# Optimization experiments

Hardware: AMD Instinct MI355X
Metric: run time of the kernel (lower is better)

Reference implementation:

```python
import jax, jax.numpy as jnp
import numpy as np

B, S, D, H = 4, 2048, 1024, 16
DK = D // H

def setup_inputs() -> dict:
    key = jax.random.key(0)
    ks = jax.random.split(key, 5)
    std = np.sqrt(2.0 / (D + D)).astype(np.float32)
    return {
        "x": jax.random.normal(ks[0], (B, S, D), dtype=jnp.float32),
        "W_q": jax.random.normal(ks[1], (D, D), dtype=jnp.float32) * std,
        "W_k": jax.random.normal(ks[2], (D, D), dtype=jnp.float32) * std,
        "W_v": jax.random.normal(ks[3], (D, D), dtype=jnp.float32) * std,
        "W_o": jax.random.normal(ks[4], (D, D), dtype=jnp.float32) * std,
    }

def reference(x, W_q, W_k, W_v, W_o):
    b, s, d = x.shape
    # Linear layers: y = x @ W.T  (W stored as [out, in])
    q = (x @ W_q.T).reshape(b, s, H, DK).transpose(0, 2, 1, 3)  # [b,h,s,dk]
    k = (x @ W_k.T).reshape(b, s, H, DK).transpose(0, 2, 1, 3)
    v = (x @ W_v.T).reshape(b, s, H, DK).transpose(0, 2, 1, 3)
    scale = 1.0 / jnp.sqrt(jnp.asarray(DK, dtype=x.dtype))
    scores = jnp.einsum("bhqd,bhkd->bhqk", q, k) * scale  # [b,h,s,s]
    causal = jnp.tril(jnp.ones((s, s), dtype=bool))
    scores = jnp.where(causal, scores, jnp.asarray(-jnp.inf, dtype=scores.dtype))
    attn = jax.nn.softmax(scores, axis=-1)
    out = jnp.einsum("bhqk,bhkd->bhqd", attn, v)  # [b,h,s,dk]
    out = out.transpose(0, 2, 1, 3).reshape(b, s, d)
    return out @ W_o.T
```

## Files before the change

### kernel.cpp

```cpp
#include <hip/hip_runtime.h>
#include <stdint.h>

#define B_  4
#define S_  2048
#define D_  1024
#define H_  16
#define DK_ 64
#define M_  (B_ * S_)

typedef __attribute__((ext_vector_type(4))) float  f32x4;
typedef __attribute__((ext_vector_type(8))) __bf16 bf16x8;
typedef __attribute__((ext_vector_type(4))) unsigned short us4;

__device__ __forceinline__ unsigned short cvt_bf16(float f) {
  unsigned u = __float_as_uint(f);
  return (unsigned short)((u + 0x7fffu + ((u >> 16) & 1u)) >> 16);
}

__device__ __forceinline__ f32x4 mfma16(bf16x8 a, bf16x8 b, f32x4 c) {
  return __builtin_amdgcn_mfma_f32_16x16x32_bf16(a, b, c, 0, 0, 0);
}

__device__ __forceinline__ void async16(const void* g, void* l) {
  __builtin_amdgcn_global_load_lds(
      (const __attribute__((address_space(1))) void*)g,
      (__attribute__((address_space(3))) void*)l, 16, 0, 0);
}

__global__ void cast_f32_bf16(const float* __restrict__ in,
                              unsigned short* __restrict__ out, int n4) {
  int i = blockIdx.x * blockDim.x + threadIdx.x;
  if (i >= n4) return;
  f32x4 v = ((const f32x4*)in)[i];
  us4 o;
  o[0] = cvt_bf16(v[0]); o[1] = cvt_bf16(v[1]);
  o[2] = cvt_bf16(v[2]); o[3] = cvt_bf16(v[3]);
  ((us4*)out)[i] = o;
}

template <int OUTMODE>
__global__ __launch_bounds__(256) void gemm_bt(
    const unsigned short* __restrict__ A,
    const unsigned short* __restrict__ Bm,
    void* __restrict__ Cp, int Mdim, int Ndim, int Kdim) {
  constexpr int BM = 128, BN = 128, BK = 32;
  __shared__ __align__(16) unsigned short As[BM * BK];
  __shared__ __align__(16) unsigned short Bs[BN * BK];

  const int tid = threadIdx.x;
  const int w = tid >> 6, l = tid & 63;
  const int l16 = l & 15, lg = l >> 4;
  const int wr = w >> 1, wc = w & 1;
  const int rowA0 = blockIdx.y * BM;
  const int rowB0 = blockIdx.x * BN;
  const int l4 = l >> 2;
  const int lk = (l & 3) * 8;

  f32x4 acc[4][4] = {};

  for (int kt = 0; kt < Kdim; kt += BK) {
#pragma unroll
    for (int j = 0; j < 2; ++j) {
      const int chunk = j * 4 + w;
      const int r = chunk * 16 + l4;
      async16(A  + (size_t)(rowA0 + r) * Kdim + kt + lk, &As[chunk * 512]);
      async16(Bm + (size_t)(rowB0 + r) * Kdim + kt + lk, &Bs[chunk * 512]);
    }
    __syncthreads();
    bf16x8 af[4], bfr[4];
#pragma unroll
    for (int m = 0; m < 4; ++m)
      af[m] = *(const bf16x8*)&As[(wr * 64 + m * 16 + l16) * BK + lg * 8];
#pragma unroll
    for (int n = 0; n < 4; ++n)
      bfr[n] = *(const bf16x8*)&Bs[(wc * 64 + n * 16 + l16) * BK + lg * 8];
#pragma unroll
    for (int m = 0; m < 4; ++m)
#pragma unroll
      for (int n = 0; n < 4; ++n)
        acc[m][n] = mfma16(af[m], bfr[n], acc[m][n]);
    __syncthreads();
  }

  const int rb = rowA0 + wr * 64;
  const int cb = rowB0 + wc * 64;
  if constexpr (OUTMODE == 2) {
    float* C = (float*)Cp;
#pragma unroll
    for (int m = 0; m < 4; ++m)
#pragma unroll
      for (int n = 0; n < 4; ++n) {
        const int r0 = rb + m * 16 + lg * 4;
        const int c0 = cb + n * 16 + l16;
#pragma unroll
        for (int j = 0; j < 4; ++j)
          C[(size_t)(r0 + j) * Ndim + c0] = acc[m][n][j];
      }
  } else if constexpr (OUTMODE == 0) {
    unsigned short* C = (unsigned short*)Cp;
#pragma unroll
    for (int m = 0; m < 4; ++m)
#pragma unroll
      for (int n = 0; n < 4; ++n) {
        const int r0 = rb + m * 16 + lg * 4;
        const int c0 = cb + n * 16 + l16;
#pragma unroll
        for (int j = 0; j < 4; ++j)
          C[(size_t)(r0 + j) * Ndim + c0] = cvt_bf16(acc[m][n][j]);
      }
  } else {
    unsigned short* C = (unsigned short*)Cp;
#pragma unroll
    for (int m = 0; m < 4; ++m)
#pragma unroll
      for (int n = 0; n < 4; ++n) {
        const int r0 = rb + m * 16 + lg * 4;
        const int c0 = cb + n * 16 + l16;
        us4 v;
#pragma unroll
        for (int j = 0; j < 4; ++j) v[j] = cvt_bf16(acc[m][n][j]);
        *(us4*)&C[((size_t)(r0 >> 11) * 1024 + c0) * 2048 + (r0 & 2047)] = v;
      }
  }
}


#define SMX(sc, mr, sr, oa, P, diag, rb, kv0)                                \
  do {                                                                       \
    _Pragma("unroll") for (int nc_ = 0; nc_ < 4; ++nc_)                      \
        _Pragma("unroll") for (int j_ = 0; j_ < 4; ++j_)                     \
            sc[nc_][j_] *= 0.125f;                                           \
    if (diag) {                                                              \
      _Pragma("unroll") for (int nc_ = 0; nc_ < 4; ++nc_) {                  \
        const int col_ = (kv0) + nc_ * 16 + l16;                             \
        _Pragma("unroll") for (int j_ = 0; j_ < 4; ++j_)                     \
            if (col_ > (rb) + j_) sc[nc_][j_] = -INFINITY;                   \
      }                                                                      \
    }                                                                        \
    _Pragma("unroll") for (int j_ = 0; j_ < 4; ++j_) {                       \
      float t_ = fmaxf(fmaxf(sc[0][j_], sc[1][j_]),                          \
                       fmaxf(sc[2][j_], sc[3][j_]));                         \
      t_ = fmaxf(t_, __shfl_xor(t_, 1));                                     \
      t_ = fmaxf(t_, __shfl_xor(t_, 2));                                     \
      t_ = fmaxf(t_, __shfl_xor(t_, 4));                                     \
      t_ = fmaxf(t_, __shfl_xor(t_, 8));                                     \
      const float mnew_ = fmaxf(mr[j_], t_);                                 \
      float rs_ = 0.f;                                                       \
      _Pragma("unroll") for (int nc_ = 0; nc_ < 4; ++nc_) {                  \
        const float p_ = __expf(sc[nc_][j_] - mnew_);                        \
        rs_ += p_;                                                           \
        P[lg * 4 + j_][nc_ * 16 + l16] = cvt_bf16(p_);                       \
      }                                                                      \
      rs_ += __shfl_xor(rs_, 1);                                             \
      rs_ += __shfl_xor(rs_, 2);                                             \
      rs_ += __shfl_xor(rs_, 4);                                             \
      rs_ += __shfl_xor(rs_, 8);                                             \
      const float al_ = __expf(mr[j_] - mnew_);                              \
      sr[j_] = sr[j_] * al_ + rs_;                                           \
      mr[j_] = mnew_;                                                        \
      _Pragma("unroll") for (int d_ = 0; d_ < 4; ++d_) oa[d_][j_] *= al_;    \
    }                                                                        \
  } while (0)

__global__ __launch_bounds__(256, 4) void flash_attn(
    const unsigned short* __restrict__ Q,
    const unsigned short* __restrict__ K,
    const unsigned short* __restrict__ Vt,
    unsigned short* __restrict__ O) {
  const int bid  = blockIdx.x;
  const int virt = (bid & 7) * 128 + (bid >> 3);
  const int bh   = virt >> 4;
  const int x    = virt & 15;
  const int b = bh >> 4, h = bh & 15;
  const int tid = threadIdx.x;
  const int w = tid >> 6, l = tid & 63;
  const int l16 = l & 15, lg = l >> 4;

  __shared__ __align__(16) unsigned short Ks[64 * 64];
  __shared__ __align__(16) unsigned short Vs[64 * 64];
  __shared__ __align__(16) unsigned short PA[4][16][72];
  __shared__ __align__(16) unsigned short PB[4][16][72];

  const int tA = x, tB = 31 - x;

  const size_t qkbase = (size_t)(b * S_) * D_ + h * DK_;
  const size_t vbase  = ((size_t)(b * D_) + h * DK_) * S_;

  const int rA = tA * 64 + w * 16 + l16;
  const int rB = tB * 64 + w * 16 + l16;
  bf16x8 qfA[2], qfB[2];
  qfA[0] = *(const bf16x8*)&Q[qkbase + (size_t)rA * D_ + lg * 8];
  qfA[1] = *(const bf16x8*)&Q[qkbase + (size_t)rA * D_ + 32 + lg * 8];
  qfB[0] = *(const bf16x8*)&Q[qkbase + (size_t)rB * D_ + lg * 8];
  qfB[1] = *(const bf16x8*)&Q[qkbase + (size_t)rB * D_ + 32 + lg * 8];

  float mA[4], sA[4], mB[4], sB[4];
  f32x4 oA[4] = {}, oB[4] = {};
#pragma unroll
  for (int j = 0; j < 4; ++j) {
    mA[j] = mB[j] = -INFINITY;
    sA[j] = sB[j] = 0.f;
  }

  const int rbA = tA * 64 + w * 16 + lg * 4;
  const int rbB = tB * 64 + w * 16 + lg * 4;

  for (int kv = 0; kv <= tB; ++kv) {
    const int kv0 = kv * 64;
    if (kv) __syncthreads();
#pragma unroll
    for (int c = 0; c < 2; ++c) {
      const int ci = c * 256 + w * 64;
      const int i  = ci + l;
      const int r  = i >> 3;
      const int cc = (i & 7) ^ (r & 7);
      async16(K  + qkbase + (size_t)(kv0 + r) * D_ + cc * 8, &Ks[ci * 8]);
      async16(Vt + vbase  + (size_t)r * S_ + kv0 + cc * 8,   &Vs[ci * 8]);
    }
    __syncthreads();

    if (kv <= tA) {
      f32x4 sc[4] = {};
#pragma unroll
      for (int nc = 0; nc < 4; ++nc) {
        const int r = nc * 16 + l16;
#pragma unroll
        for (int ks = 0; ks < 2; ++ks) {
          const int byte = (r * 128 + ks * 64 + lg * 16) ^ ((r & 7) << 4);
          bf16x8 kf = *(const bf16x8*)((const char*)Ks + byte);
          sc[nc] = mfma16(qfA[ks], kf, sc[nc]);
        }
      }
      SMX(sc, mA, sA, oA, PA[w], kv == tA, rbA, kv0);
      __asm__ volatile("s_waitcnt lgkmcnt(0)" ::: "memory");
      bf16x8 pa0 = *(const bf16x8*)&PA[w][l16][lg * 8];
      bf16x8 pa1 = *(const bf16x8*)&PA[w][l16][32 + lg * 8];
#pragma unroll
      for (int d = 0; d < 4; ++d) {
        const int r = d * 16 + l16;
#pragma unroll
        for (int ks = 0; ks < 2; ++ks) {
          const int byte = (r * 128 + ks * 64 + lg * 16) ^ ((r & 7) << 4);
          bf16x8 vf = *(const bf16x8*)((const char*)Vs + byte);
          oA[d] = mfma16(ks ? pa1 : pa0, vf, oA[d]);
        }
      }
    }

    {
      f32x4 sc[4] = {};
#pragma unroll
      for (int nc = 0; nc < 4; ++nc) {
        const int r = nc * 16 + l16;
#pragma unroll
        for (int ks = 0; ks < 2; ++ks) {
          const int byte = (r * 128 + ks * 64 + lg * 16) ^ ((r & 7) << 4);
          bf16x8 kf = *(const bf16x8*)((const char*)Ks + byte);
          sc[nc] = mfma16(qfB[ks], kf, sc[nc]);
        }
      }
      SMX(sc, mB, sB, oB, PB[w], kv == tB, rbB, kv0);
      __asm__ volatile("s_waitcnt lgkmcnt(0)" ::: "memory");
      bf16x8 pb0 = *(const bf16x8*)&PB[w][l16][lg * 8];
      bf16x8 pb1 = *(const bf16x8*)&PB[w][l16][32 + lg * 8];
#pragma unroll
      for (int d = 0; d < 4; ++d) {
        const int r = d * 16 + l16;
#pragma unroll
        for (int ks = 0; ks < 2; ++ks) {
          const int byte = (r * 128 + ks * 64 + lg * 16) ^ ((r & 7) << 4);
          bf16x8 vf = *(const bf16x8*)((const char*)Vs + byte);
          oB[d] = mfma16(ks ? pb1 : pb0, vf, oB[d]);
        }
      }
    }
  }

#pragma unroll
  for (int d = 0; d < 4; ++d)
#pragma unroll
    for (int j = 0; j < 4; ++j) {
      O[((size_t)(b * S_) + rbA + j) * D_ + h * DK_ + d * 16 + l16] =
          cvt_bf16(oA[d][j] / sA[j]);
      O[((size_t)(b * S_) + rbB + j) * D_ + h * DK_ + d * 16 + l16] =
          cvt_bf16(oB[d][j] / sB[j]);
    }
}

extern "C" void kernel_launch(void* const* d_in, const int* in_sizes, int n_in,
                              void* d_out, int out_size, void* d_ws,
                              size_t ws_size, hipStream_t stream) {
  const float* x  = (const float*)d_in[0];
  const float* Wq = (const float*)d_in[1];
  const float* Wk = (const float*)d_in[2];
  const float* Wv = (const float*)d_in[3];
  const float* Wo = (const float*)d_in[4];

  const size_t XN = (size_t)M_ * D_;
  const size_t WN = (size_t)D_ * D_;
  unsigned short* xb  = (unsigned short*)d_ws;
  unsigned short* Wqb = xb + XN;
  unsigned short* Wkb = Wqb + WN;
  unsigned short* Wvb = Wkb + WN;
  unsigned short* Wob = Wvb + WN;
  unsigned short* Qb  = Wob + WN;
  unsigned short* Kb  = Qb + XN;
  unsigned short* Vtb = Kb + XN;
  unsigned short* Ob  = Vtb + XN;

  cast_f32_bf16<<<(int)(XN / 4 / 256), 256, 0, stream>>>(x, xb, (int)(XN / 4));
  cast_f32_bf16<<<(int)(WN / 4 / 256), 256, 0, stream>>>(Wq, Wqb, (int)(WN / 4));
  cast_f32_bf16<<<(int)(WN / 4 / 256), 256, 0, stream>>>(Wk, Wkb, (int)(WN / 4));
  cast_f32_bf16<<<(int)(WN / 4 / 256), 256, 0, stream>>>(Wv, Wvb, (int)(WN / 4));
  cast_f32_bf16<<<(int)(WN / 4 / 256), 256, 0, stream>>>(Wo, Wob, (int)(WN / 4));

  dim3 gg(D_ / 128, M_ / 128);
  gemm_bt<0><<<gg, 256, 0, stream>>>(xb, Wqb, Qb, M_, D_, D_);
  gemm_bt<0><<<gg, 256, 0, stream>>>(xb, Wkb, Kb, M_, D_, D_);
  gemm_bt<1><<<gg, 256, 0, stream>>>(xb, Wvb, Vtb, M_, D_, D_);

  flash_attn<<<dim3(1024), 256, 0, stream>>>(Qb, Kb, Vtb, Ob);

  gemm_bt<2><<<gg, 256, 0, stream>>>(Ob, Wob, d_out, M_, D_, D_);
}
```

Measured before the change: 346.9 us.

## Fuse casts and QKV GEMMs, skip softmax rescale, use exp2 and setprio

Merges the five cast kernels into one launch and fuses the Q/K/V projections into a single GEMM over the concatenated weight matrix (N=3072), with the output routed per region. In flash attention, the 1/sqrt(dk) scale is folded into an exp2 constant, the rescale of the accumulator is skipped when the row max does not change (wave-uniform check), MFMA sections get raised wave priority, and the final division becomes a reciprocal multiply. The intent is to cut launch overhead, reuse x loads across the three projections, and trim softmax ALU work. The cost is extra branching and slightly different rounding.

```diff
diff --git a/kernel.cpp b/kernel.cpp
--- a/kernel.cpp
+++ b/kernel.cpp
@@ -27,22 +27,40 @@
       (__attribute__((address_space(3))) void*)l, 16, 0, 0);
 }
 
-__global__ void cast_f32_bf16(const float* __restrict__ in,
-                              unsigned short* __restrict__ out, int n4) {
-  int i = blockIdx.x * blockDim.x + threadIdx.x;
-  if (i >= n4) return;
-  f32x4 v = ((const f32x4*)in)[i];
+#define XN4_ 2097152
+#define WN4_ 262144
+__global__ void cast_all(const float* __restrict__ x,
+                         const float* __restrict__ wq,
+                         const float* __restrict__ wk,
+                         const float* __restrict__ wv,
+                         const float* __restrict__ wo,
+                         unsigned short* __restrict__ dst) {
+  const int i = blockIdx.x * blockDim.x + threadIdx.x;
+  const float* src;
+  int k;
+  if (i < XN4_) {
+    src = x; k = i;
+  } else {
+    const int j = i - XN4_;
+    const int wsel = j >> 18;
+    k = j & (WN4_ - 1);
+    src = (wsel == 0) ? wq : (wsel == 1) ? wk : (wsel == 2) ? wv : wo;
+  }
+  f32x4 v = ((const f32x4*)src)[k];
   us4 o;
   o[0] = cvt_bf16(v[0]); o[1] = cvt_bf16(v[1]);
   o[2] = cvt_bf16(v[2]); o[3] = cvt_bf16(v[3]);
-  ((us4*)out)[i] = o;
+  ((us4*)dst)[i] = o;
 }
 
 template <int OUTMODE>
 __global__ __launch_bounds__(256) void gemm_bt(
     const unsigned short* __restrict__ A,
     const unsigned short* __restrict__ Bm,
-    void* __restrict__ Cp, int Mdim, int Ndim, int Kdim) {
+    void* __restrict__ Cp,
+    unsigned short* __restrict__ Qo, unsigned short* __restrict__ Ko,
+    unsigned short* __restrict__ Vto,
+    int Ndim, int Kdim) {
   constexpr int BM = 128, BN = 128, BK = 32;
   __shared__ __align__(16) unsigned short As[BM * BK];
   __shared__ __align__(16) unsigned short Bs[BN * BK];
@@ -96,40 +114,42 @@
         for (int j = 0; j < 4; ++j)
           C[(size_t)(r0 + j) * Ndim + c0] = acc[m][n][j];
       }
-  } else if constexpr (OUTMODE == 0) {
-    unsigned short* C = (unsigned short*)Cp;
-#pragma unroll
-    for (int m = 0; m < 4; ++m)
-#pragma unroll
-      for (int n = 0; n < 4; ++n) {
-        const int r0 = rb + m * 16 + lg * 4;
-        const int c0 = cb + n * 16 + l16;
-#pragma unroll
-        for (int j = 0; j < 4; ++j)
-          C[(size_t)(r0 + j) * Ndim + c0] = cvt_bf16(acc[m][n][j]);
-      }
   } else {
-    unsigned short* C = (unsigned short*)Cp;
-#pragma unroll
-    for (int m = 0; m < 4; ++m)
-#pragma unroll
-      for (int n = 0; n < 4; ++n) {
-        const int r0 = rb + m * 16 + lg * 4;
-        const int c0 = cb + n * 16 + l16;
-        us4 v;
-#pragma unroll
-        for (int j = 0; j < 4; ++j) v[j] = cvt_bf16(acc[m][n][j]);
-        *(us4*)&C[((size_t)(r0 >> 11) * 1024 + c0) * 2048 + (r0 & 2047)] = v;
-      }
-  }
-}
-
+    const int region = cb >> 10;
+    const int cbl = cb & 1023;
+    if (region < 2) {
+      unsigned short* C = region ? Ko : Qo;
+#pragma unroll
+      for (int m = 0; m < 4; ++m)
+#pragma unroll
+        for (int n = 0; n < 4; ++n) {
+          const int r0 = rb + m * 16 + lg * 4;
+          const int c0 = cbl + n * 16 + l16;
+#pragma unroll
+          for (int j = 0; j < 4; ++j)
+            C[(size_t)(r0 + j) * 1024 + c0] = cvt_bf16(acc[m][n][j]);
+        }
+    } else {
+#pragma unroll
+      for (int m = 0; m < 4; ++m)
+#pragma unroll
+        for (int n = 0; n < 4; ++n) {
+          const int r0 = rb + m * 16 + lg * 4;
+          const int c0 = cbl + n * 16 + l16;
+          us4 v;
+#pragma unroll
+          for (int j = 0; j < 4; ++j) v[j] = cvt_bf16(acc[m][n][j]);
+          *(us4*)&Vto[((size_t)(r0 >> 11) * 1024 + c0) * 2048 + (r0 & 2047)] = v;
+        }
+    }
+  }
+}
+
+
+#define KS_ 0.1803368801f
 
 #define SMX(sc, mr, sr, oa, P, diag, rb, kv0)                                \
   do {                                                                       \
-    _Pragma("unroll") for (int nc_ = 0; nc_ < 4; ++nc_)                      \
-        _Pragma("unroll") for (int j_ = 0; j_ < 4; ++j_)                     \
-            sc[nc_][j_] *= 0.125f;                                           \
     if (diag) {                                                              \
       _Pragma("unroll") for (int nc_ = 0; nc_ < 4; ++nc_) {                  \
         const int col_ = (kv0) + nc_ * 16 + l16;                             \
@@ -144,10 +164,11 @@
       t_ = fmaxf(t_, __shfl_xor(t_, 2));                                     \
       t_ = fmaxf(t_, __shfl_xor(t_, 4));                                     \
       t_ = fmaxf(t_, __shfl_xor(t_, 8));                                     \
-      const float mnew_ = fmaxf(mr[j_], t_);                                 \
+      const bool st_ = __all(t_ <= mr[j_]);     \
+      const float mnew_ = st_ ? mr[j_] : fmaxf(mr[j_], t_);                  \
       float rs_ = 0.f;                                                       \
       _Pragma("unroll") for (int nc_ = 0; nc_ < 4; ++nc_) {                  \
-        const float p_ = __expf(sc[nc_][j_] - mnew_);                        \
+        const float p_ = exp2f((sc[nc_][j_] - mnew_) * KS_);                 \
         rs_ += p_;                                                           \
         P[lg * 4 + j_][nc_ * 16 + l16] = cvt_bf16(p_);                       \
       }                                                                      \
@@ -155,10 +176,14 @@
       rs_ += __shfl_xor(rs_, 2);                                             \
       rs_ += __shfl_xor(rs_, 4);                                             \
       rs_ += __shfl_xor(rs_, 8);                                             \
-      const float al_ = __expf(mr[j_] - mnew_);                              \
-      sr[j_] = sr[j_] * al_ + rs_;                                           \
-      mr[j_] = mnew_;                                                        \
-      _Pragma("unroll") for (int d_ = 0; d_ < 4; ++d_) oa[d_][j_] *= al_;    \
+      if (st_) {                                                             \
+        sr[j_] += rs_;                                                       \
+      } else {                                                               \
+        const float al_ = exp2f((mr[j_] - mnew_) * KS_);                     \
+        sr[j_] = sr[j_] * al_ + rs_;                                         \
+        mr[j_] = mnew_;                                                      \
+        _Pragma("unroll") for (int d_ = 0; d_ < 4; ++d_) oa[d_][j_] *= al_;  \
+      }                                                                      \
     }                                                                        \
   } while (0)
 
@@ -221,6 +246,7 @@
 
     if (kv <= tA) {
       f32x4 sc[4] = {};
+      __builtin_amdgcn_s_setprio(1);
 #pragma unroll
       for (int nc = 0; nc < 4; ++nc) {
         const int r = nc * 16 + l16;
@@ -231,10 +257,12 @@
           sc[nc] = mfma16(qfA[ks], kf, sc[nc]);
         }
       }
+      __builtin_amdgcn_s_setprio(0);
       SMX(sc, mA, sA, oA, PA[w], kv == tA, rbA, kv0);
       __asm__ volatile("s_waitcnt lgkmcnt(0)" ::: "memory");
       bf16x8 pa0 = *(const bf16x8*)&PA[w][l16][lg * 8];
       bf16x8 pa1 = *(const bf16x8*)&PA[w][l16][32 + lg * 8];
+      __builtin_amdgcn_s_setprio(1);
 #pragma unroll
       for (int d = 0; d < 4; ++d) {
         const int r = d * 16 + l16;
@@ -245,10 +273,12 @@
           oA[d] = mfma16(ks ? pa1 : pa0, vf, oA[d]);
         }
       }
+      __builtin_amdgcn_s_setprio(0);
     }
 
     {
       f32x4 sc[4] = {};
+      __builtin_amdgcn_s_setprio(1);
 #pragma unroll
       for (int nc = 0; nc < 4; ++nc) {
         const int r = nc * 16 + l16;
@@ -259,10 +289,12 @@
           sc[nc] = mfma16(qfB[ks], kf, sc[nc]);
         }
       }
+      __builtin_amdgcn_s_setprio(0);
       SMX(sc, mB, sB, oB, PB[w], kv == tB, rbB, kv0);
       __asm__ volatile("s_waitcnt lgkmcnt(0)" ::: "memory");
       bf16x8 pb0 = *(const bf16x8*)&PB[w][l16][lg * 8];
       bf16x8 pb1 = *(const bf16x8*)&PB[w][l16][32 + lg * 8];
+      __builtin_amdgcn_s_setprio(1);
 #pragma unroll
       for (int d = 0; d < 4; ++d) {
         const int r = d * 16 + l16;
@@ -273,18 +305,22 @@
           oB[d] = mfma16(ks ? pb1 : pb0, vf, oB[d]);
         }
       }
-    }
-  }
-
-#pragma unroll
-  for (int d = 0; d < 4; ++d)
-#pragma unroll
-    for (int j = 0; j < 4; ++j) {
+      __builtin_amdgcn_s_setprio(0);
+    }
+  }
+
+#pragma unroll
+  for (int j = 0; j < 4; ++j) {
+    const float iA = __builtin_amdgcn_rcpf(sA[j]);
+    const float iB = __builtin_amdgcn_rcpf(sB[j]);
+#pragma unroll
+    for (int d = 0; d < 4; ++d) {
       O[((size_t)(b * S_) + rbA + j) * D_ + h * DK_ + d * 16 + l16] =
-          cvt_bf16(oA[d][j] / sA[j]);
+          cvt_bf16(oA[d][j] * iA);
       O[((size_t)(b * S_) + rbB + j) * D_ + h * DK_ + d * 16 + l16] =
-          cvt_bf16(oB[d][j] / sB[j]);
-    }
+          cvt_bf16(oB[d][j] * iB);
+    }
+  }
 }
 
 extern "C" void kernel_launch(void* const* d_in, const int* in_sizes, int n_in,
@@ -300,26 +336,19 @@
   const size_t WN = (size_t)D_ * D_;
   unsigned short* xb  = (unsigned short*)d_ws;
   unsigned short* Wqb = xb + XN;
-  unsigned short* Wkb = Wqb + WN;
-  unsigned short* Wvb = Wkb + WN;
-  unsigned short* Wob = Wvb + WN;
+  unsigned short* Wob = Wqb + 3 * WN;
   unsigned short* Qb  = Wob + WN;
   unsigned short* Kb  = Qb + XN;
   unsigned short* Vtb = Kb + XN;
   unsigned short* Ob  = Vtb + XN;
 
-  cast_f32_bf16<<<(int)(XN / 4 / 256), 256, 0, stream>>>(x, xb, (int)(XN / 4));
-  cast_f32_bf16<<<(int)(WN / 4 / 256), 256, 0, stream>>>(Wq, Wqb, (int)(WN / 4));
-  cast_f32_bf16<<<(int)(WN / 4 / 256), 256, 0, stream>>>(Wk, Wkb, (int)(WN / 4));
-  cast_f32_bf16<<<(int)(WN / 4 / 256), 256, 0, stream>>>(Wv, Wvb, (int)(WN / 4));
-  cast_f32_bf16<<<(int)(WN / 4 / 256), 256, 0, stream>>>(Wo, Wob, (int)(WN / 4));
-
-  dim3 gg(D_ / 128, M_ / 128);
-  gemm_bt<0><<<gg, 256, 0, stream>>>(xb, Wqb, Qb, M_, D_, D_);
-  gemm_bt<0><<<gg, 256, 0, stream>>>(xb, Wkb, Kb, M_, D_, D_);
-  gemm_bt<1><<<gg, 256, 0, stream>>>(xb, Wvb, Vtb, M_, D_, D_);
+  cast_all<<<(XN4_ + 4 * WN4_) / 256, 256, 0, stream>>>(x, Wq, Wk, Wv, Wo, xb);
+
+  gemm_bt<3><<<dim3(24, 64), 256, 0, stream>>>(xb, Wqb, nullptr, Qb, Kb, Vtb,
+                                               3072, D_);
 
   flash_attn<<<dim3(1024), 256, 0, stream>>>(Qb, Kb, Vtb, Ob);
 
-  gemm_bt<2><<<gg, 256, 0, stream>>>(Ob, Wob, d_out, M_, D_, D_);
-}
+  gemm_bt<2><<<dim3(8, 64), 256, 0, stream>>>(Ob, Wob, d_out, nullptr, nullptr,
+                                              nullptr, D_, D_);
+}
```

After: 318.2 us. 8.3% less time.
